# Performance work log

Hardware: AMD Instinct MI355X
Metric: run time of the kernel (lower is better)

## Reference

```python
import jax, jax.numpy as jnp
import numpy as np

B, D = 32, 2048


def setup_inputs() -> dict:
    key = jax.random.key(0)
    ks = jax.random.split(key, 7)
    # torch init: weights ~ N(0, 0.1^2); biases default Linear uniform(-1/sqrt(D), 1/sqrt(D))
    bound = 1.0 / np.sqrt(D)
    return {
        "x": jax.random.normal(ks[0], (B, D), dtype=jnp.float32),
        "Wq": 0.1 * jax.random.normal(ks[1], (D, D), dtype=jnp.float32),
        "bq": jax.random.uniform(ks[2], (D,), minval=-bound, maxval=bound, dtype=jnp.float32),
        "Wk": 0.1 * jax.random.normal(ks[3], (D, D), dtype=jnp.float32),
        "bk": jax.random.uniform(ks[4], (D,), minval=-bound, maxval=bound, dtype=jnp.float32),
        "Wv": 0.1 * jax.random.normal(ks[5], (D, D), dtype=jnp.float32),
        "bv": jax.random.uniform(ks[6], (D,), minval=-bound, maxval=bound, dtype=jnp.float32),
    }


def reference(x, Wq, bq, Wk, bk, Wv, bv):
    # q,k,v: [B, D] feature-wise projections (torch Linear: x @ W^T + b)
    q = x @ Wq.T + bq
    k = x @ Wk.T + bk
    v = x @ Wv.T + bv
    # rank-1 outer product scores[b,i,j] = q[b,i] * k[b,j]  -> [B, D, D]
    scores = q[:, :, None] * k[:, None, :]
    # softmax over dim=1 (as in the original F.softmax(..., dim=1))
    weights = jax.nn.softmax(scores, axis=1)
    # weighted V sum: out[b,i] = sum_j weights[b,i,j] * v[b,j]  -> [B, D]
    out = jnp.einsum("bij,bj->bi", weights, v)
    return out
```

## Files before the change

kernel.cpp:

```cpp
#include <hip/hip_runtime.h>
#include <math.h>


#define D 2048
#define BATCH 32

#define PART_STRIDE 196608
#define BQV_OFF   786432
#define BQI_OFF   851968
#define BK2_OFF   917504
#define BKI_OFF   983040
#define META_OFF  1048576
#define PKD_OFF   1051136
#define NPT_OFF   1182208
#define SMETA_OFF 1184256

#define L2E 1.4426950408889634f

typedef short s16x8 __attribute__((ext_vector_type(8)));
typedef float f32x4 __attribute__((ext_vector_type(4)));

union FragU { s16x8 v; unsigned u[4]; };

__device__ __forceinline__ float fast_exp2(float x) {
#if __has_builtin(__builtin_amdgcn_exp2f)
  return __builtin_amdgcn_exp2f(x);
#else
  return exp2f(x);
#endif
}
__device__ __forceinline__ int bits_below(unsigned long long m) {
  return __builtin_amdgcn_mbcnt_hi((unsigned)(m >> 32),
         __builtin_amdgcn_mbcnt_lo((unsigned)m, 0));
}
__device__ __forceinline__ unsigned pack_rne(float a, float b) {
  unsigned ua = __float_as_uint(a), ub = __float_as_uint(b);
  ua = ua + 0x7FFFu + ((ua >> 16) & 1u);
  ub = ub + 0x7FFFu + ((ub >> 16) & 1u);
  return (ua >> 16) | (ub & 0xFFFF0000u);
}
__device__ __forceinline__ void pack8(const float4& fa, const float4& fb,
                                      FragU& h) {
  h.u[0] = pack_rne(fa.x, fa.y);
  h.u[1] = pack_rne(fa.z, fa.w);
  h.u[2] = pack_rne(fb.x, fb.y);
  h.u[3] = pack_rne(fb.z, fb.w);
}
__device__ __forceinline__ float sum_parts(const float* __restrict__ ws,
                                           size_t o) {
  float s0 = ws[o] + ws[o + PART_STRIDE];
  float s1 = ws[o + 2 * PART_STRIDE] + ws[o + 3 * PART_STRIDE];
  return s0 + s1;
}

__global__ __launch_bounds__(256, 2) void k1_proj(
    const float* __restrict__ x, const float* __restrict__ Wq,
    const float* __restrict__ Wk, const float* __restrict__ Wv,
    float* __restrict__ ws) {
  __shared__ float red[4][512];
  const int tid = threadIdx.x;
  const int lane = tid & 63, wv = tid >> 6;
  const int tile = blockIdx.x >> 2, kq = blockIdx.x & 3;
  const int m = tile >> 7, lr = (tile & 127) * 16;
  const float* W = (m == 0) ? Wq : (m == 1) ? Wk : Wv;

  const int kbase = kq * 512 + wv * 128 + (lane >> 4) * 8;
  const float* ap = W + (size_t)(lr + (lane & 15)) * D + kbase;
  const float* xp0 = x + (size_t)(lane & 15) * D + kbase;
  const float* xp1 = xp0 + 16 * D;

  float4 fa[4], fb[4], x0a[4], x0b[4], x1a[4], x1b[4];
#pragma unroll
  for (int s = 0; s < 4; ++s) {
    const int off = s * 32;
    fa[s] = *(const float4*)(ap + off);
    fb[s] = *(const float4*)(ap + off + 4);
    x0a[s] = *(const float4*)(xp0 + off);
    x0b[s] = *(const float4*)(xp0 + off + 4);
    x1a[s] = *(const float4*)(xp1 + off);
    x1b[s] = *(const float4*)(xp1 + off + 4);
  }

  f32x4 acc0 = {0.f, 0.f, 0.f, 0.f}, acc1 = {0.f, 0.f, 0.f, 0.f};
#pragma unroll
  for (int s = 0; s < 4; ++s) {
    FragU Ah, Bh0, Bh1;
    pack8(fa[s], fb[s], Ah);
    pack8(x0a[s], x0b[s], Bh0);
    pack8(x1a[s], x1b[s], Bh1);
    acc0 = __builtin_amdgcn_mfma_f32_16x16x32_bf16(Ah.v, Bh0.v, acc0, 0, 0, 0);
    acc1 = __builtin_amdgcn_mfma_f32_16x16x32_bf16(Ah.v, Bh1.v, acc1, 0, 0, 0);
  }
  const int col = lane & 15, rq = (lane >> 4) * 4;
#pragma unroll
  for (int r = 0; r < 4; ++r) {
    red[wv][col * 16 + rq + r] = acc0[r];
    red[wv][(col + 16) * 16 + rq + r] = acc1[r];
  }
  __syncthreads();
  float* part = ws + (size_t)kq * PART_STRIDE + (size_t)m * 65536;
#pragma unroll
  for (int i = tid; i < 512; i += 256) {
    float s = (red[0][i] + red[1][i]) + (red[2][i] + red[3][i]);
    part[(size_t)(i >> 4) * D + lr + (i & 15)] = s;
  }
}

__global__ __launch_bounds__(512) void k0_prep(float* __restrict__ ws,
                                               const float* __restrict__ bq,
                                               const float* __restrict__ bk) {
  __shared__ int cnt[64], off[65], cur[64];
  __shared__ float rmx[8], rmn[8];
  const int bx = blockIdx.x, t = threadIdx.x;
  const int b = bx & 31, pass = bx >> 5;
  const size_t qb = (size_t)b * D;
  float* meta = ws + META_OFF + b * 80;

  const size_t src = (pass ? 65536 : 0) + qb;
  float4 p0 = ((const float4*)(ws + src))[t];
  float4 p1 = ((const float4*)(ws + PART_STRIDE + src))[t];
  float4 p2 = ((const float4*)(ws + 2 * PART_STRIDE + src))[t];
  float4 p3 = ((const float4*)(ws + 3 * PART_STRIDE + src))[t];
  float4 bb = pass ? ((const float4*)bk)[t] : ((const float4*)bq)[t];
  float4 qv = {(p0.x + p1.x) + (p2.x + p3.x) + bb.x,
               (p0.y + p1.y) + (p2.y + p3.y) + bb.y,
               (p0.z + p1.z) + (p2.z + p3.z) + bb.z,
               (p0.w + p1.w) + (p2.w + p3.w) + bb.w};
  if (pass) {
    qv.x *= L2E; qv.y *= L2E; qv.z *= L2E; qv.w *= L2E;
  }
  float mx = fmaxf(fmaxf(qv.x, qv.y), fmaxf(qv.z, qv.w));
  float mn = fminf(fminf(qv.x, qv.y), fminf(qv.z, qv.w));
#pragma unroll
  for (int o = 32; o; o >>= 1) {
    mx = fmaxf(mx, __shfl_down(mx, o));
    mn = fminf(mn, __shfl_down(mn, o));
  }
  if ((t & 63) == 0) { rmx[t >> 6] = mx; rmn[t >> 6] = mn; }
  if (t < 64) cnt[t] = 0;
  __syncthreads();
  mx = rmx[0]; mn = rmn[0];
#pragma unroll
  for (int w = 1; w < 8; ++w) {
    mx = fmaxf(mx, rmx[w]);
    mn = fminf(mn, rmn[w]);
  }
  const float scale = (mx > mn) ? 64.0f / (mx - mn) : 0.f;
  float vals[4] = {qv.x, qv.y, qv.z, qv.w};
  int bi[4];
#pragma unroll
  for (int e = 0; e < 4; ++e) {
    bi[e] = (int)fminf(63.f, fmaxf(0.f, (vals[e] - mn) * scale));
    atomicAdd(&cnt[bi[e]], 1);
  }
  __syncthreads();
  if (t == 0) {
    int a = 0;
#pragma unroll
    for (int i = 0; i < 64; ++i) { off[i] = a; cur[i] = a; a += cnt[i]; }
    off[64] = a;
  }
  __syncthreads();
  const size_t vdst = (pass ? BK2_OFF : BQV_OFF) + qb;
  const size_t idst = (pass ? BKI_OFF : BQI_OFF) + qb;
#pragma unroll
  for (int e = 0; e < 4; ++e) {
    const int pos = atomicAdd(&cur[bi[e]], 1);
    ws[vdst + pos] = vals[e];
    ((int*)ws)[idst + pos] = t * 4 + e;
  }
  if (pass == 0) {
    if (t == 0) { meta[0] = mx; meta[1] = mn; meta[2] = scale; }
    if (t < 65) ((int*)meta)[8 + t] = off[t];
  }
}

__global__ __launch_bounds__(512, 8) void k3_z(float* __restrict__ ws,
                                               const float* __restrict__ bv) {
  __shared__ float qs[2048];
  __shared__ float zs[512];
  __shared__ int ob[65];
  const int bx = blockIdx.x, t = threadIdx.x;
  const int b = bx & 31, s = bx >> 5;
  const int g = (s & 1) ? 32 + (s >> 1) : 31 - (s >> 1);
  const size_t qb = (size_t)b * D;
  const float* meta = ws + META_OFF + b * 80;

  ((float4*)qs)[t] = ((const float4*)(ws + BQV_OFF + qb))[t];
  if (t < 65) ob[t] = ((const int*)meta)[8 + t];
  const float qmx = meta[0], qmn = meta[1], scale = meta[2];

  const int jl = t & 31, ih = t >> 5;
  const int p = g * 32 + jl;
  const float k2 = ws[BK2_OFF + qb + p];
  const int oj = ((const int*)ws)[BKI_OFF + qb + p];
  const float m2 = (k2 >= 0.f) ? k2 * qmx : k2 * qmn;
  const float nm2 = -m2;
  const float k2lo = __shfl(k2, 0);
  const float k2hi = __shfl(k2, 31);
  __syncthreads();

  int st, en;
  if (k2lo >= 0.f) {
    const float c = qmx - 40.f / k2lo;
    const int B = (int)fminf(63.f, fmaxf(0.f, (c - qmn) * scale));
    st = ob[B] & ~3; en = 2048;
  } else if (k2hi < 0.f) {
    const float c = qmn + 40.f / (-k2hi);
    const int B = (int)fminf(63.f, fmaxf(0.f, (c - qmn) * scale));
    st = 0; en = (ob[B + 1] + 3) & ~3;
  } else {
    st = 0; en = 2048;
  }
  const int nq = (en - st) >> 2;
  const int i0 = st + (((nq * ih) >> 4) << 2);
  const int i1 = st + (((nq * (ih + 1)) >> 4) << 2);
  float z0 = 0.f, z1 = 0.f, z2 = 0.f, z3 = 0.f;
  for (int idx = i0; idx < i1; idx += 4) {
    float4 q4 = *(const float4*)&qs[idx];
    z0 += fast_exp2(fmaf(q4.x, k2, nm2));
    z1 += fast_exp2(fmaf(q4.y, k2, nm2));
    z2 += fast_exp2(fmaf(q4.z, k2, nm2));
    z3 += fast_exp2(fmaf(q4.w, k2, nm2));
  }
  zs[ih * 32 + jl] = (z0 + z1) + (z2 + z3);
  __syncthreads();

  if (t < 32) {
    float Z = 0.f;
#pragma unroll
    for (int h = 0; h < 16; ++h) Z += zs[h * 32 + t];
    const float v = sum_parts(ws, 131072 + qb + oj) + bv[oj];
    const float d = __log2f(fabsf(v) / Z) - m2;
    const unsigned long long msk = __ballot(v >= 0.f);
    const int npos = __popcll(msk);
    const int slot = (v >= 0.f) ? bits_below(msk)
                                : 31 - bits_below(~msk & 0xFFFFFFFFull);
    float2* dst = (float2*)(ws + PKD_OFF) + ((size_t)b * 64 + g) * 32;
    dst[slot] = make_float2(k2, d);
    if (t == 0) ((int*)(ws + NPT_OFF))[b * 64 + g] = npos;
    float kmn = k2, kmx = k2, dmx = d;
#pragma unroll
    for (int o = 16; o; o >>= 1) {
      kmn = fminf(kmn, __shfl_down(kmn, o, 32));
      kmx = fmaxf(kmx, __shfl_down(kmx, o, 32));
      dmx = fmaxf(dmx, __shfl_down(dmx, o, 32));
    }
    if (t == 0)
      ((float4*)(ws + SMETA_OFF))[b * 64 + g] =
          make_float4(kmn, kmx, dmx, 0.f);
  }
}

__global__ __launch_bounds__(512, 8) void k4_out(const float* __restrict__ ws,
                                                 float* __restrict__ out) {
  __shared__ float2 kd[2048];
  __shared__ float4 sm[64];
  __shared__ int np[64];
  __shared__ float rs[64 * 9];
  const int bx = blockIdx.x, t = threadIdx.x;
  const int b = bx & 31, s = bx >> 5;
  const int ic = (s & 1) ? 31 - (s >> 1) : (s >> 1);
  const size_t qb = (size_t)b * D;

  const float4* src = (const float4*)((const float2*)(ws + PKD_OFF) +
                                      (size_t)b * 2048);
  ((float4*)kd)[t] = src[t];
  ((float4*)kd)[t + 512] = src[t + 512];
  if (t < 64) {
    np[t] = ((const int*)(ws + NPT_OFF))[b * 64 + t];
    sm[t] = ((const float4*)(ws + SMETA_OFF))[b * 64 + t];
  }
  const int il = t & 63, jh = t >> 6;
  const int pos = ic * 64 + il;
  const float qi = ws[BQV_OFF + qb + pos];
  const int oi = ((const int*)ws)[BQI_OFF + qb + pos];
  __syncthreads();

  float p0 = 0.f, p1 = 0.f, p2 = 0.f, p3 = 0.f;
  float n0 = 0.f, n1 = 0.f, n2 = 0.f, n3 = 0.f;
#pragma unroll
  for (int s8 = 0; s8 < 8; ++s8) {
    const int sg = jh * 8 + s8;
    const float4 m = sm[sg];
    const float ub = fmaxf(m.x * qi, m.y * qi) + m.z;
    if (__all(ub < -28.f)) continue;
    const float4* seg = (const float4*)(kd + sg * 32);
    const int npos = np[sg], gb = npos >> 2;
    for (int gq = 0; gq < gb; ++gq) {
      float4 a = seg[gq * 2], c = seg[gq * 2 + 1];
      p0 += fast_exp2(fmaf(qi, a.x, a.y));
      p1 += fast_exp2(fmaf(qi, a.z, a.w));
      p2 += fast_exp2(fmaf(qi, c.x, c.y));
      p3 += fast_exp2(fmaf(qi, c.z, c.w));
    }
    if (gb < 8) {
      {
        float4 a = seg[gb * 2], c = seg[gb * 2 + 1];
        const int base = gb * 4;
        float e0 = fast_exp2(fmaf(qi, a.x, a.y));
        float e1 = fast_exp2(fmaf(qi, a.z, a.w));
        float e2 = fast_exp2(fmaf(qi, c.x, c.y));
        float e3 = fast_exp2(fmaf(qi, c.z, c.w));
        if (base + 0 < npos) p0 += e0; else n0 += e0;
        if (base + 1 < npos) p1 += e1; else n1 += e1;
        if (base + 2 < npos) p2 += e2; else n2 += e2;
        if (base + 3 < npos) p3 += e3; else n3 += e3;
      }
      for (int gq = gb + 1; gq < 8; ++gq) {
        float4 a = seg[gq * 2], c = seg[gq * 2 + 1];
        n0 += fast_exp2(fmaf(qi, a.x, a.y));
        n1 += fast_exp2(fmaf(qi, a.z, a.w));
        n2 += fast_exp2(fmaf(qi, c.x, c.y));
        n3 += fast_exp2(fmaf(qi, c.z, c.w));
      }
    }
  }
  rs[il * 9 + jh] = ((p0 + p1) + (p2 + p3)) - ((n0 + n1) + (n2 + n3));
  __syncthreads();
  if (t < 64) {
    float sum = 0.f;
#pragma unroll
    for (int h = 0; h < 8; ++h) sum += rs[t * 9 + h];
    out[qb + oi] = sum;
  }
}

extern "C" void kernel_launch(void* const* d_in, const int* in_sizes, int n_in,
                              void* d_out, int out_size, void* d_ws, size_t ws_size,
                              hipStream_t stream) {
  (void)in_sizes; (void)n_in; (void)out_size; (void)ws_size;
  const float* x  = (const float*)d_in[0];
  const float* Wq = (const float*)d_in[1];
  const float* bq = (const float*)d_in[2];
  const float* bk = (const float*)d_in[4];
  const float* Wk = (const float*)d_in[3];
  const float* Wv = (const float*)d_in[5];
  const float* bv = (const float*)d_in[6];
  float* ws  = (float*)d_ws;
  float* out = (float*)d_out;

  k1_proj<<<1536, 256, 0, stream>>>(x, Wq, Wk, Wv, ws);
  k0_prep<<<64, 512, 0, stream>>>(ws, bq, bk);
  k3_z<<<2048, 512, 0, stream>>>(ws, bv);
  k4_out<<<1024, 512, 0, stream>>>(ws, out);
}
```

Baseline: 134.4 us.

## Fuse output accumulation into the Z kernel using per-group atomics

Merges k4_out into k3_z. Each block now computes its own 32-key group's (k, d) pairs into shared memory, then loops over the 64-wide query chunks that survive a group-level bound check and atomically adds its partial sums into the output. The output is zeroed inside k1_proj. This removes one kernel launch and the global round trip for the packed key metadata, and skips inactive chunks per group. In exchange it adds 64 float atomics per output element, which makes the summation order nondeterministic, and puts more work and shared memory on k3.

```diff
diff --git a/kernel.cpp b/kernel.cpp
--- a/kernel.cpp
+++ b/kernel.cpp
@@ -11,9 +11,6 @@
 #define BK2_OFF   917504
 #define BKI_OFF   983040
 #define META_OFF  1048576
-#define PKD_OFF   1051136
-#define NPT_OFF   1182208
-#define SMETA_OFF 1184256
 
 #define L2E 1.4426950408889634f
 
@@ -56,9 +53,10 @@
 __global__ __launch_bounds__(256, 2) void k1_proj(
     const float* __restrict__ x, const float* __restrict__ Wq,
     const float* __restrict__ Wk, const float* __restrict__ Wv,
-    float* __restrict__ ws) {
+    float* __restrict__ ws, float* __restrict__ out) {
   __shared__ float red[4][512];
   const int tid = threadIdx.x;
+  if (blockIdx.x < 256) out[(blockIdx.x << 8) + tid] = 0.f;
   const int lane = tid & 63, wv = tid >> 6;
   const int tile = blockIdx.x >> 2, kq = blockIdx.x & 3;
   const int m = tile >> 7, lr = (tile & 127) * 16;
@@ -126,9 +124,7 @@
                (p0.y + p1.y) + (p2.y + p3.y) + bb.y,
                (p0.z + p1.z) + (p2.z + p3.z) + bb.z,
                (p0.w + p1.w) + (p2.w + p3.w) + bb.w};
-  if (pass) {
-    qv.x *= L2E; qv.y *= L2E; qv.z *= L2E; qv.w *= L2E;
-  }
+  if (pass) { qv.x *= L2E; qv.y *= L2E; qv.z *= L2E; qv.w *= L2E; }
   float mx = fmaxf(fmaxf(qv.x, qv.y), fmaxf(qv.z, qv.w));
   float mn = fminf(fminf(qv.x, qv.y), fminf(qv.z, qv.w));
 #pragma unroll
@@ -175,18 +171,35 @@
   }
 }
 
-__global__ __launch_bounds__(512, 8) void k3_z(float* __restrict__ ws,
-                                               const float* __restrict__ bv) {
+__global__ __launch_bounds__(512, 8) void k3_out(float* __restrict__ ws,
+                                                 const float* __restrict__ bv,
+                                                 float* __restrict__ out) {
   __shared__ float qs[2048];
+  __shared__ int qix[2048];
   __shared__ float zs[512];
   __shared__ int ob[65];
+  __shared__ float cmn[32], cmx[32];
+  __shared__ float2 kdl[32];
+  __shared__ float gmeta[3];
+  __shared__ int gint[2];
+  __shared__ int actl[32];
   const int bx = blockIdx.x, t = threadIdx.x;
   const int b = bx & 31, s = bx >> 5;
   const int g = (s & 1) ? 32 + (s >> 1) : 31 - (s >> 1);
   const size_t qb = (size_t)b * D;
   const float* meta = ws + META_OFF + b * 80;
 
-  ((float4*)qs)[t] = ((const float4*)(ws + BQV_OFF + qb))[t];
+  const float4 qv4 = ((const float4*)(ws + BQV_OFF + qb))[t];
+  ((float4*)qs)[t] = qv4;
+  ((int4*)qix)[t] = ((const int4*)((const int*)ws + BQI_OFF + qb))[t];
+  float cl = fminf(fminf(qv4.x, qv4.y), fminf(qv4.z, qv4.w));
+  float ch = fmaxf(fmaxf(qv4.x, qv4.y), fmaxf(qv4.z, qv4.w));
+#pragma unroll
+  for (int o = 1; o < 16; o <<= 1) {
+    cl = fminf(cl, __shfl_xor(cl, o));
+    ch = fmaxf(ch, __shfl_xor(ch, o));
+  }
+  if ((t & 15) == 0) { cmn[t >> 4] = cl; cmx[t >> 4] = ch; }
   if (t < 65) ob[t] = ((const int*)meta)[8 + t];
   const float qmx = meta[0], qmn = meta[1], scale = meta[2];
 
@@ -233,62 +246,48 @@
     const float v = sum_parts(ws, 131072 + qb + oj) + bv[oj];
     const float d = __log2f(fabsf(v) / Z) - m2;
     const unsigned long long msk = __ballot(v >= 0.f);
-    const int npos = __popcll(msk);
+    const int np_ = __popcll(msk);
     const int slot = (v >= 0.f) ? bits_below(msk)
                                 : 31 - bits_below(~msk & 0xFFFFFFFFull);
-    float2* dst = (float2*)(ws + PKD_OFF) + ((size_t)b * 64 + g) * 32;
-    dst[slot] = make_float2(k2, d);
-    if (t == 0) ((int*)(ws + NPT_OFF))[b * 64 + g] = npos;
-    float kmn = k2, kmx = k2, dmx = d;
+    kdl[slot] = make_float2(k2, d);
+    float kmn_ = k2, kmx_ = k2, dmx_ = d;
 #pragma unroll
     for (int o = 16; o; o >>= 1) {
-      kmn = fminf(kmn, __shfl_down(kmn, o, 32));
-      kmx = fmaxf(kmx, __shfl_down(kmx, o, 32));
-      dmx = fmaxf(dmx, __shfl_down(dmx, o, 32));
+      kmn_ = fminf(kmn_, __shfl_down(kmn_, o, 32));
+      kmx_ = fmaxf(kmx_, __shfl_down(kmx_, o, 32));
+      dmx_ = fmaxf(dmx_, __shfl_down(dmx_, o, 32));
     }
-    if (t == 0)
-      ((float4*)(ws + SMETA_OFF))[b * 64 + g] =
-          make_float4(kmn, kmx, dmx, 0.f);
-  }
-}
-
-__global__ __launch_bounds__(512, 8) void k4_out(const float* __restrict__ ws,
-                                                 float* __restrict__ out) {
-  __shared__ float2 kd[2048];
-  __shared__ float4 sm[64];
-  __shared__ int np[64];
-  __shared__ float rs[64 * 9];
-  const int bx = blockIdx.x, t = threadIdx.x;
-  const int b = bx & 31, s = bx >> 5;
-  const int ic = (s & 1) ? 31 - (s >> 1) : (s >> 1);
-  const size_t qb = (size_t)b * D;
-
-  const float4* src = (const float4*)((const float2*)(ws + PKD_OFF) +
-                                      (size_t)b * 2048);
-  ((float4*)kd)[t] = src[t];
-  ((float4*)kd)[t + 512] = src[t + 512];
-  if (t < 64) {
-    np[t] = ((const int*)(ws + NPT_OFF))[b * 64 + t];
-    sm[t] = ((const float4*)(ws + SMETA_OFF))[b * 64 + t];
-  }
+    if (t == 0) {
+      gmeta[0] = kmn_; gmeta[1] = kmx_; gmeta[2] = dmx_;
+      gint[0] = np_;
+    }
+  }
+  __syncthreads();
+
+  const float kmn = gmeta[0], kmx = gmeta[1], dmx = gmeta[2];
+  const int npos = gint[0];
+  if (t < 32) {
+    const float a = cmn[t], c = cmx[t];
+    const float bnd = fmaxf(fmaxf(kmn * a, kmx * a),
+                            fmaxf(kmn * c, kmx * c)) + dmx;
+    const unsigned long long am = __ballot(bnd >= -28.f);
+    if (bnd >= -28.f) actl[bits_below(am)] = t;
+    if (t == 0) gint[1] = __popcll(am);
+  }
+  __syncthreads();
+  const int nact = gint[1];
   const int il = t & 63, jh = t >> 6;
-  const int pos = ic * 64 + il;
-  const float qi = ws[BQV_OFF + qb + pos];
-  const int oi = ((const int*)ws)[BQI_OFF + qb + pos];
-  __syncthreads();
-
-  float p0 = 0.f, p1 = 0.f, p2 = 0.f, p3 = 0.f;
-  float n0 = 0.f, n1 = 0.f, n2 = 0.f, n3 = 0.f;
-#pragma unroll
-  for (int s8 = 0; s8 < 8; ++s8) {
-    const int sg = jh * 8 + s8;
-    const float4 m = sm[sg];
-    const float ub = fmaxf(m.x * qi, m.y * qi) + m.z;
-    if (__all(ub < -28.f)) continue;
-    const float4* seg = (const float4*)(kd + sg * 32);
-    const int npos = np[sg], gb = npos >> 2;
+  const int gb = npos >> 2;
+  const float4* kd4 = (const float4*)kdl;
+  for (int bs = jh; bs < nact; bs += 8) {
+    const int ca = actl[bs];
+    const int pos = ca * 64 + il;
+    const float qi = qs[pos];
+    const int oi = qix[pos];
+    float p0 = 0.f, p1 = 0.f, p2 = 0.f, p3 = 0.f;
+    float n0 = 0.f, n1 = 0.f, n2 = 0.f, n3 = 0.f;
     for (int gq = 0; gq < gb; ++gq) {
-      float4 a = seg[gq * 2], c = seg[gq * 2 + 1];
+      float4 a = kd4[gq * 2], c = kd4[gq * 2 + 1];
       p0 += fast_exp2(fmaf(qi, a.x, a.y));
       p1 += fast_exp2(fmaf(qi, a.z, a.w));
       p2 += fast_exp2(fmaf(qi, c.x, c.y));
@@ -296,7 +295,7 @@
     }
     if (gb < 8) {
       {
-        float4 a = seg[gb * 2], c = seg[gb * 2 + 1];
+        float4 a = kd4[gb * 2], c = kd4[gb * 2 + 1];
         const int base = gb * 4;
         float e0 = fast_exp2(fmaf(qi, a.x, a.y));
         float e1 = fast_exp2(fmaf(qi, a.z, a.w));
@@ -308,21 +307,16 @@
         if (base + 3 < npos) p3 += e3; else n3 += e3;
       }
       for (int gq = gb + 1; gq < 8; ++gq) {
-        float4 a = seg[gq * 2], c = seg[gq * 2 + 1];
+        float4 a = kd4[gq * 2], c = kd4[gq * 2 + 1];
         n0 += fast_exp2(fmaf(qi, a.x, a.y));
         n1 += fast_exp2(fmaf(qi, a.z, a.w));
         n2 += fast_exp2(fmaf(qi, c.x, c.y));
         n3 += fast_exp2(fmaf(qi, c.z, c.w));
       }
     }
-  }
-  rs[il * 9 + jh] = ((p0 + p1) + (p2 + p3)) - ((n0 + n1) + (n2 + n3));
-  __syncthreads();
-  if (t < 64) {
-    float sum = 0.f;
-#pragma unroll
-    for (int h = 0; h < 8; ++h) sum += rs[t * 9 + h];
-    out[qb + oi] = sum;
+    const float sres =
+        ((p0 + p1) + (p2 + p3)) - ((n0 + n1) + (n2 + n3));
+    atomicAdd(&out[qb + oi], sres);
   }
 }
 
@@ -333,15 +327,14 @@
   const float* x  = (const float*)d_in[0];
   const float* Wq = (const float*)d_in[1];
   const float* bq = (const float*)d_in[2];
+  const float* Wk = (const float*)d_in[3];
   const float* bk = (const float*)d_in[4];
-  const float* Wk = (const float*)d_in[3];
   const float* Wv = (const float*)d_in[5];
   const float* bv = (const float*)d_in[6];
   float* ws  = (float*)d_ws;
   float* out = (float*)d_out;
 
-  k1_proj<<<1536, 256, 0, stream>>>(x, Wq, Wk, Wv, ws);
+  k1_proj<<<1536, 256, 0, stream>>>(x, Wq, Wk, Wv, ws, out);
   k0_prep<<<64, 512, 0, stream>>>(ws, bq, bk);
-  k3_z<<<2048, 512, 0, stream>>>(ws, bv);
-  k4_out<<<1024, 512, 0, stream>>>(ws, out);
-}
+  k3_out<<<2048, 512, 0, stream>>>(ws, bv, out);
+}
```

Measured after the change: 177.5 us. 32.1% more time.
